# Kernel optimization log

Hardware: AMD Instinct MI355X
Metric: run time of the kernel (lower is better)

The kernel has to match this reference:

```python
import jax, jax.numpy as jnp
import numpy as np

T, B, H = 1024, 128, 256


def setup_inputs() -> dict:
    key = jax.random.key(0)
    k1, k2, k3, k4, k5 = jax.random.split(key, 5)
    ins = jax.random.normal(k1, (T, B, H), dtype=jnp.float32)
    resets = jax.random.randint(k2, (T, B), 0, 2).astype(jnp.bool_)
    # GRUCell params (flax layout): input dense (with bias) and recurrent dense
    # (bias only on the candidate 'hn' branch). Orthogonal-ish init approximated
    # by scaled normal for a pure-jnp reference.
    s = 1.0 / np.sqrt(H)
    Wi = jax.random.normal(k3, (H, 3 * H), dtype=jnp.float32) * s   # -> [ir|iz|in]
    Wh = jax.random.normal(k4, (H, 3 * H), dtype=jnp.float32) * s   # -> [hr|hz|hn]
    bi = jnp.zeros((3 * H,), dtype=jnp.float32)
    bhn = jnp.zeros((H,), dtype=jnp.float32)
    h0 = jnp.zeros((B, H), dtype=jnp.float32)  # initialize_carry -> zeros
    return {"ins": ins, "resets": resets, "h0": h0,
            "Wi": Wi, "Wh": Wh, "bi": bi, "bhn": bhn}


def reference(ins, resets, h0, Wi, Wh, bi, bhn):
    """ScannedRNN: GRU recurrence over time with per-step reset masking.

    ins: [T,B,H], resets: [T,B] bool, h0: [B,H]. Returns (final_carry, ys).
    """
    Hh = h0.shape[-1]

    def step(h, xt):
        x_t, r_t = xt                              # [B,H], [B]
        h = jnp.where(r_t[:, None], 0.0, h)        # reset carry to zeros
        gi = x_t @ Wi + bi                         # [B,3H]
        gh = h @ Wh                                # [B,3H]
        i_r, i_z, i_n = gi[:, :Hh], gi[:, Hh:2 * Hh], gi[:, 2 * Hh:]
        h_r, h_z, h_n = gh[:, :Hh], gh[:, Hh:2 * Hh], gh[:, 2 * Hh:]
        r = jax.nn.sigmoid(i_r + h_r)
        z = jax.nn.sigmoid(i_z + h_z)
        n = jnp.tanh(i_n + r * (h_n + bhn))
        h_new = (1.0 - z) * n + z * h
        return h_new, h_new                        # GRUCell returns (carry, y=carry)

    h_final, ys = jax.lax.scan(step, h0, (ins, resets))
    return h_final, ys
```

## Files before the change

### kernel.cpp

```cpp
#include <hip/hip_runtime.h>


typedef _Float16 half2_t __attribute__((ext_vector_type(2)));
typedef _Float16 half4_t __attribute__((ext_vector_type(4)));
typedef _Float16 half8_t __attribute__((ext_vector_type(8)));
typedef float f32x4 __attribute__((ext_vector_type(4)));

#define T_DIM 1024
#define B_DIM 128
#define H_DIM 256
#define N3 768
#define NSTREAM 8192
#define ROWS 16

__device__ __forceinline__ int perm_n(int cp) {
  int ublk = cp / 48;
  int rem = cp % 48;
  int g = rem >> 4;
  int u4 = rem & 15;
  return g * 256 + ublk * 16 + u4;
}


__global__ void prep_whb(const float* __restrict__ Wh, unsigned* __restrict__ WhB) {
  int i = blockIdx.x * 256 + threadIdx.x;
  int h = 2 * i;
  int idx = h & 7;
  int lane = (h >> 3) & 63;
  int ntk = h >> 9;
  int nt = ntk % 48;
  int kt = ntk / 48;
  int k = kt * 32 + ((lane >> 4) * 8) + idx;
  int n = perm_n(nt * 16 + (lane & 15));
  half2_t p;
  p.x = (_Float16)Wh[(size_t)k * N3 + n];
  p.y = (_Float16)Wh[(size_t)(k + 1) * N3 + n];
  WhB[i] = __builtin_bit_cast(unsigned, p);
}

__global__ void prep_witp(const float* __restrict__ Wi, _Float16* __restrict__ WiTp) {
  int i = blockIdx.x * 256 + threadIdx.x;
  int cp = i >> 8;
  int k = i & 255;
  WiTp[(size_t)cp * 256 + k] = (_Float16)Wi[(size_t)k * N3 + perm_n(cp)];
}

__global__ void prep_bip(const float* __restrict__ bi, float* __restrict__ bip) {
  int i = threadIdx.x;
  bip[i] = bi[perm_n(i)];
}

__global__ void init_h(const float* __restrict__ h0, float* __restrict__ h_state) {
  int i = blockIdx.x * 256 + threadIdx.x;
  h_state[i] = h0[i];
}

__global__ __launch_bounds__(256) void conv_a(
    const float* __restrict__ src, _Float16* __restrict__ dst, int n8) {
  int i = blockIdx.x * 256 + threadIdx.x;
  const int stride = gridDim.x * 256;
  for (; i < n8; i += stride) {
    float4 a = ((const float4*)src)[2 * i];
    float4 b = ((const float4*)src)[2 * i + 1];
    half8_t h;
    h[0] = (_Float16)a.x; h[1] = (_Float16)a.y;
    h[2] = (_Float16)a.z; h[3] = (_Float16)a.w;
    h[4] = (_Float16)b.x; h[5] = (_Float16)b.y;
    h[6] = (_Float16)b.z; h[7] = (_Float16)b.w;
    ((half8_t*)dst)[i] = h;
  }
}


__global__ void seg_transpose(const int* __restrict__ resets, int* __restrict__ resT) {
  int i = blockIdx.x * 256 + threadIdx.x;
  int b = i >> 10;
  int t = i & 1023;
  resT[i] = resets[(size_t)t * B_DIM + b];
}

__global__ __launch_bounds__(256) void seg_extract(
    const int* __restrict__ resT, int t0, int steps,
    unsigned* __restrict__ rowsegs, unsigned* __restrict__ rowcnt,
    unsigned* __restrict__ lhist) {
  const int b = blockIdx.x;
  const int tid = threadIdx.x;
  const int lane = tid & 63;
  const int w = tid >> 6;
  const int per = (steps + 255) >> 8;

  __shared__ unsigned short sstartL[1025];
  __shared__ unsigned lcur[1025];
  __shared__ unsigned wsum[4];

  for (int l = tid; l <= steps; l += 256) lcur[l] = 0;

  const int* rrow = resT + (size_t)b * T_DIM + t0;
  int myfirst = tid * per;
  unsigned cnt = 0;
  for (int i = 0; i < per; ++i) {
    int s = myfirst + i;
    if (s < steps && (s == 0 || rrow[s] != 0)) cnt++;
  }
  unsigned pre = cnt;
#pragma unroll
  for (int off = 1; off < 64; off <<= 1) {
    unsigned v = __shfl_up(pre, off);
    if (lane >= off) pre += v;
  }
  if (lane == 63) wsum[w] = pre;
  __syncthreads();
  unsigned wbase = 0, total = 0;
#pragma unroll
  for (int i = 0; i < 4; ++i) {
    if (i < w) wbase += wsum[i];
    total += wsum[i];
  }
  unsigned r = wbase + pre - cnt;
  for (int i = 0; i < per; ++i) {
    int s = myfirst + i;
    if (s < steps && (s == 0 || rrow[s] != 0)) sstartL[r++] = (unsigned short)s;
  }
  if (tid == 0) { sstartL[total] = (unsigned short)steps; rowcnt[b] = total; }
  __syncthreads();

  const unsigned carry0 = (rrow[0] == 0) ? 1u : 0u;
  for (unsigned rr = tid; rr < total; rr += 256) {
    int st = sstartL[rr];
    int len = (int)sstartL[rr + 1] - st;
    unsigned carry = (st == 0) ? carry0 : 0u;
    unsigned rk = atomicAdd(&lcur[len], 1u);
    rowsegs[(size_t)b * T_DIM + rr] =
        (unsigned)st | ((unsigned)len << 10) | (rk << 21) | (carry << 31);
  }
  __syncthreads();
  for (int l = tid; l <= steps; l += 256) lhist[(size_t)l * 128 + b] = lcur[l];
}

__global__ __launch_bounds__(1024) void seg_prefix2(
    const unsigned* __restrict__ lhist, unsigned* __restrict__ rowoff,
    unsigned* __restrict__ cursors, unsigned* __restrict__ Warr,
    unsigned* __restrict__ nseg, int steps) {
  __shared__ unsigned cs[1024];
  __shared__ unsigned cs2[1024];
  const int tid = threadIdx.x;
  const int len = tid + 1;
  unsigned run = 0;
  if (len <= steps) {
    for (int b = 0; b < 128; ++b) {
      rowoff[(size_t)len * 128 + b] = run;
      run += lhist[(size_t)len * 128 + b];
    }
  }
  unsigned own = run;
  unsigned own2 = run * (unsigned)len;
  cs[tid] = own;
  cs2[tid] = own2;
  for (int off = 1; off < 1024; off <<= 1) {
    __syncthreads();
    unsigned v = (tid + off < 1024) ? cs[tid + off] : 0u;
    unsigned v2 = (tid + off < 1024) ? cs2[tid + off] : 0u;
    __syncthreads();
    cs[tid] += v;
    cs2[tid] += v2;
  }
  cursors[len] = cs[tid] - own;
  Warr[len] = cs2[tid] - own2;
  if (tid == 0) *nseg = cs[0];
}

__global__ void seg_scatter2(
    const unsigned* __restrict__ rowsegs, const unsigned* __restrict__ rowcnt,
    const unsigned* __restrict__ rowoff, const unsigned* __restrict__ cursors,
    unsigned* __restrict__ segs) {
  int i = blockIdx.x * 256 + threadIdx.x;
  int b = i >> 10;
  int rr = i & 1023;
  if ((unsigned)rr >= rowcnt[b]) return;
  unsigned rec = rowsegs[i];
  unsigned st = rec & 0x3FF;
  unsigned len = (rec >> 10) & 0x7FF;
  unsigned rk = (rec >> 21) & 0x3FF;
  unsigned carry = rec >> 31;
  unsigned dst = cursors[len] + rowoff[(size_t)len * 128 + b] + rk;
  segs[dst] = st | (len << 10) | ((unsigned)b << 21) | (carry << 28);
}

__global__ void str_mark(
    const unsigned* __restrict__ segs, const unsigned* __restrict__ nseg_p,
    const unsigned* __restrict__ cursors, const unsigned* __restrict__ Warr,
    unsigned* __restrict__ sstart, unsigned* __restrict__ preexS, int Q) {
  unsigned r = blockIdx.x * 256 + threadIdx.x;
  unsigned n = *nseg_p;
  if (r >= n) return;
  unsigned rec = segs[r];
  unsigned len = (rec >> 10) & 0x7FF;
  unsigned pre = Warr[len] + len * (r - cursors[len]);
  unsigned st = pre / (unsigned)Q;
  unsigned stp;
  if (r == 0) {
    sstart[0] = 0; preexS[0] = 0; stp = 0;
  } else {
    unsigned rec2 = segs[r - 1];
    unsigned len2 = (rec2 >> 10) & 0x7FF;
    unsigned pre2 = Warr[len2] + len2 * (r - 1 - cursors[len2]);
    stp = pre2 / (unsigned)Q;
  }
  for (unsigned s = stp + 1; s <= st; ++s) { sstart[s] = r; preexS[s] = pre; }
}

__global__ __launch_bounds__(256) void gi_gemm(
    const _Float16* __restrict__ A16,
    const _Float16* __restrict__ BT,
    const float* __restrict__ bip,
    _Float16* __restrict__ Cout,
    int M) {
  __shared__ _Float16 Al[128 * 32];
  __shared__ _Float16 Bl[128 * 32];
  const int tid = threadIdx.x;
  const int lane = tid & 63;
  const int w = tid >> 6;
  const int wr = w >> 1, wc = w & 1;
  const int m0 = blockIdx.y * 128;
  const int n0 = blockIdx.x * 128;

  const int srow = lane >> 2;
  const int schunk = lane & 3;

  f32x4 acc[4][4] = {};

  for (int ks = 0; ks < 256; ks += 32) {
#pragma unroll
    for (int rr = 0; rr < 2; ++rr) {
      const int row = w * 32 + rr * 16;
      __builtin_amdgcn_global_load_lds(
          (const __attribute__((address_space(1))) void*)
              ((const char*)A16 + ((size_t)(m0 + row + srow) * 256 + ks) * 2 + schunk * 16),
          (__attribute__((address_space(3))) void*)((char*)Al + row * 64),
          16, 0, 0);
      __builtin_amdgcn_global_load_lds(
          (const __attribute__((address_space(1))) void*)
              ((const char*)BT + ((size_t)(n0 + row + srow) * 256 + ks) * 2 + schunk * 16),
          (__attribute__((address_space(3))) void*)((char*)Bl + row * 64),
          16, 0, 0);
    }
    __syncthreads();

    half8_t af[4], bf[4];
#pragma unroll
    for (int m = 0; m < 4; ++m)
      af[m] = *(const half8_t*)&Al[(size_t)(wr * 64 + m * 16 + (lane & 15)) * 32 + (lane >> 4) * 8];
#pragma unroll
    for (int n = 0; n < 4; ++n)
      bf[n] = *(const half8_t*)&Bl[(size_t)(wc * 64 + n * 16 + (lane & 15)) * 32 + (lane >> 4) * 8];
#pragma unroll
    for (int m = 0; m < 4; ++m)
#pragma unroll
      for (int n = 0; n < 4; ++n)
        acc[m][n] = __builtin_amdgcn_mfma_f32_16x16x32_f16(af[m], bf[n], acc[m][n], 0, 0, 0);
    __syncthreads();
  }

#pragma unroll
  for (int m = 0; m < 4; ++m) {
    int row = m0 + wr * 64 + m * 16 + (lane >> 4) * 4;
#pragma unroll
    for (int n = 0; n < 4; ++n) {
      int col = n0 + wc * 64 + n * 16 + (lane & 15);
      float bv = bip[col];
#pragma unroll
      for (int r2 = 0; r2 < 4; ++r2)
        Cout[(size_t)(row + r2) * N3 + col] = (_Float16)(acc[m][n][r2] + bv);
    }
  }
}

__global__ __launch_bounds__(512)
__attribute__((amdgpu_waves_per_eu(1, 4)))
void scan_stream(
    const _Float16* __restrict__ WhB,
    const _Float16* __restrict__ gi,
    const unsigned* __restrict__ segs,
    const unsigned* __restrict__ sstart,
    const unsigned* __restrict__ preexS,
    const unsigned* __restrict__ nseg_ptr,
    const float* __restrict__ bhn,
    const float* __restrict__ h_in,
    float* __restrict__ h_out,
    float* __restrict__ ys,
    float* __restrict__ hfin,
    int t0, int steps, int Q) {
  __shared__ _Float16 h_lds[2][ROWS][264];
  __shared__ _Float16 giL[2][ROWS][776];
  __shared__ unsigned rst[ROWS];
  __shared__ unsigned rowrankL[ROWS];
  __shared__ unsigned rowpwL[ROWS];
  __shared__ unsigned wava[8];

  const int tid = threadIdx.x;
  const int lane = tid & 63;
  const int w = tid >> 6;
  const int sbase = blockIdx.x * ROWS;
  const unsigned nseg = *nseg_ptr;

  if (tid < ROWS) {
    const unsigned st = sbase + tid;
    unsigned r = sstart[st], pw = preexS[st];
    unsigned v = 0u, rk = 0xFFFFFFFFu, rpw0 = 0u;
    if (r < nseg && pw < (st + 1) * (unsigned)Q) {
      unsigned rec = segs[r];
      unsigned len = (rec >> 10) & 0x7FF;
      v = (rec & 0x3FF) | (((rec >> 21) & 0x7F) << 10) | (len << 17) |
          (((rec >> 28) & 1u) << 28);
      rk = r; rpw0 = pw + len;
    }
    rst[tid] = v; rowrankL[tid] = rk; rowpwL[tid] = rpw0;
  }
  if (tid < 8) wava[tid] = 1u;

  half8_t whr[48];
#pragma unroll
  for (int kt = 0; kt < 8; ++kt)
#pragma unroll
    for (int q = 0; q < 6; ++q)
      whr[kt * 6 + q] =
          *(const half8_t*)&WhB[(((size_t)kt * 48 + w * 6 + q) * 64 + lane) * 8];

  __syncthreads();

  unsigned rcur[2], rnxt[2], rrk[2], rpw[2], segnx[2], lim[2];
  unsigned rfr[2];
#pragma unroll
  for (int rr = 0; rr < 2; ++rr) {
    const int row = 2 * w + rr;
    rcur[rr] = rst[row];
    rrk[rr]  = rowrankL[row];
    rpw[rr]  = rowpwL[row];
    lim[rr]  = (unsigned)(sbase + row + 1) * (unsigned)Q;
    unsigned rn2 = rrk[rr] + 1;
    unsigned i2 = (rn2 < nseg) ? rn2 : (nseg - 1);
    segnx[rr] = segs[i2];
  }

#pragma unroll
  for (int rr = 0; rr < 2; ++rr) {
    int row = 2 * w + rr;
    unsigned s = rcur[rr];
    float4 o = make_float4(0.f, 0.f, 0.f, 0.f);
    if (s & (1u << 28))
      o = *(const float4*)&h_in[(size_t)((s >> 10) & 0x7F) * 256 + lane * 4];
    half4_t hv;
    hv.x = (_Float16)o.x; hv.y = (_Float16)o.y;
    hv.z = (_Float16)o.z; hv.w = (_Float16)o.w;
    *(half4_t*)&h_lds[0][row][lane * 4] = hv;
  }

#pragma unroll
  for (int rr = 0; rr < 2; ++rr) {
    const int row = 2 * w + rr;
    const unsigned ss = rcur[rr];
    if ((ss >> 17) & 0x7FF) {
      const char* src = (const char*)(gi +
          ((size_t)(ss & 0x3FF) * B_DIM + ((ss >> 10) & 0x7F)) * N3);
      char* dst = (char*)&giL[0][row][0];
#if __has_builtin(__builtin_amdgcn_global_load_lds)
      __builtin_amdgcn_global_load_lds(
          (const __attribute__((address_space(1))) void*)(src + (size_t)lane * 16),
          (__attribute__((address_space(3))) void*)dst, 16, 0, 0);
      __builtin_amdgcn_global_load_lds(
          (const __attribute__((address_space(1))) void*)(src + 1024 + (size_t)lane * 4),
          (__attribute__((address_space(3))) void*)(dst + 1024), 4, 0, 0);
      __builtin_amdgcn_global_load_lds(
          (const __attribute__((address_space(1))) void*)(src + 1280 + (size_t)lane * 4),
          (__attribute__((address_space(3))) void*)(dst + 1280), 4, 0, 0);
#else
      {
        uint4 a = *(const uint4*)(src + ((size_t)(lane & 31)) * 48);
        uint4 b = *(const uint4*)(src + ((size_t)(lane & 31)) * 48 + 16);
        uint4 c = *(const uint4*)(src + ((size_t)(lane & 31)) * 48 + 32);
        if ((lane >> 5) == 0) {
          char* d2 = dst + ((size_t)(lane & 31)) * 48;
          *(uint4*)(d2) = a; *(uint4*)(d2 + 16) = b; *(uint4*)(d2 + 32) = c;
        }
      }
#endif
    }
  }

  const int r16 = lane & 15;
  const int q4 = (lane >> 4) * 4;
  const int kq8 = (lane >> 4) * 8;
  const int u0 = w * 32 + r16;
  const float bh0 = bhn[u0];
  const float bh1 = bhn[u0 + 16];

  int cur = 0;
  int hc = 0;
  while (true) {
    asm volatile("s_waitcnt vmcnt(0)" ::: "memory");
    asm volatile("s_waitcnt lgkmcnt(0)" ::: "memory");
    __builtin_amdgcn_s_barrier();
    __builtin_amdgcn_sched_barrier(0);

    unsigned alive = 0;
#pragma unroll
    for (int i = 0; i < 8; ++i) alive += wava[i];
    if (!alive) break;

#pragma unroll
    for (int rr = 0; rr < 2; ++rr) {
      const unsigned cs = rcur[rr];
      const unsigned rem = (cs >> 17) & 0x7FF;
      unsigned nx = 0u;
      rfr[rr] = 0u;
      if (rem > 1) {
        nx = ((cs & 0x3FF) + 1) | (cs & (0x7Fu << 10)) | ((rem - 1) << 17);
      } else if (rem == 1) {
        unsigned rn = rrk[rr] + 1;
        unsigned pw = rpw[rr];
        if (rn < nseg && pw < lim[rr]) {
          unsigned rec = segnx[rr];
          unsigned len = (rec >> 10) & 0x7FF;
          nx = (rec & 0x3FF) | (((rec >> 21) & 0x7F) << 10) | (len << 17) |
               (((rec >> 28) & 1u) << 28);
          rrk[rr] = rn; rpw[rr] = pw + len;
          rfr[rr] = 1u;
          unsigned rn2 = rn + 1;
          unsigned i2 = (rn2 < nseg) ? rn2 : (nseg - 1);
          segnx[rr] = segs[i2];
        }
      }
      rnxt[rr] = nx;
    }

#pragma unroll
    for (int rr = 0; rr < 2; ++rr) {
      const int row = 2 * w + rr;
      const unsigned ss = rnxt[rr];
      if ((ss >> 17) & 0x7FF) {
        const char* src = (const char*)(gi +
            ((size_t)(ss & 0x3FF) * B_DIM + ((ss >> 10) & 0x7F)) * N3);
        char* dst = (char*)&giL[cur ^ 1][row][0];
#if __has_builtin(__builtin_amdgcn_global_load_lds)
        __builtin_amdgcn_global_load_lds(
            (const __attribute__((address_space(1))) void*)(src + (size_t)lane * 16),
            (__attribute__((address_space(3))) void*)dst, 16, 0, 0);
        __builtin_amdgcn_global_load_lds(
            (const __attribute__((address_space(1))) void*)(src + 1024 + (size_t)lane * 4),
            (__attribute__((address_space(3))) void*)(dst + 1024), 4, 0, 0);
        __builtin_amdgcn_global_load_lds(
            (const __attribute__((address_space(1))) void*)(src + 1280 + (size_t)lane * 4),
            (__attribute__((address_space(3))) void*)(dst + 1280), 4, 0, 0);
#else
        {
          uint4 a = *(const uint4*)(src + ((size_t)(lane & 31)) * 48);
          uint4 b = *(const uint4*)(src + ((size_t)(lane & 31)) * 48 + 16);
          uint4 c = *(const uint4*)(src + ((size_t)(lane & 31)) * 48 + 32);
          if ((lane >> 5) == 0) {
            char* d2 = dst + ((size_t)(lane & 31)) * 48;
            *(uint4*)(d2) = a; *(uint4*)(d2 + 16) = b; *(uint4*)(d2 + 32) = c;
          }
        }
#endif
      }
    }

    f32x4 acc[6] = {};
#pragma unroll
    for (int kt = 0; kt < 8; ++kt) {
      half8_t afr = *(const half8_t*)&h_lds[hc][r16][kt * 32 + kq8];
#pragma unroll
      for (int q = 0; q < 6; ++q)
        acc[q] = __builtin_amdgcn_mfma_f32_16x16x32_f16(afr, whr[kt * 6 + q], acc[q], 0, 0, 0);
    }

#pragma unroll
    for (int j = 0; j < 2; ++j) {
      const int u = u0 + j * 16;
      const int cb = w * 96 + j * 48 + r16;
      const float bh = j ? bh1 : bh0;
#pragma unroll
      for (int e = 0; e < 4; ++e) {
        const int row = q4 + e;
        if ((rst[row] >> 17) & 0x7FF) {
          const float gr = (float)giL[cur][row][cb];
          const float gz = (float)giL[cur][row][cb + 16];
          const float gn = (float)giL[cur][row][cb + 32];
          const float sigr = 1.f / (1.f + __expf(-(gr + acc[3 * j][e])));
          const float sigz = 1.f / (1.f + __expf(-(gz + acc[3 * j + 1][e])));
          const float narg = gn + sigr * (acc[3 * j + 2][e] + bh);
          const float eo = __expf(-2.f * narg);
          const float nn = 2.f / (1.f + eo) - 1.f;
          const float hold = (float)h_lds[hc][row][u];
          const float hnew = (1.f - sigz) * nn + sigz * hold;
          h_lds[hc ^ 1][row][u] = (_Float16)hnew;
        }
      }
    }

    asm volatile("s_waitcnt lgkmcnt(0)" ::: "memory");
    __builtin_amdgcn_s_barrier();
    __builtin_amdgcn_sched_barrier(0);

    unsigned alv = 0;
#pragma unroll
    for (int rr = 0; rr < 2; ++rr) {
      const int row = 2 * w + rr;
      const unsigned sp = rcur[rr];
      const unsigned rem = (sp >> 17) & 0x7FF;
      if (rem) {
        const int t = sp & 0x3FF;
        const int b = (sp >> 10) & 0x7F;
        half4_t hv = *(const half4_t*)&h_lds[hc ^ 1][row][lane * 4];
        float4 o;
        o.x = (float)hv.x; o.y = (float)hv.y; o.z = (float)hv.z; o.w = (float)hv.w;
        *(float4*)&ys[(((size_t)(t0 + t) * B_DIM + b) * H_DIM) + lane * 4] = o;
        if (rem == 1) {
          if (t == steps - 1) *(float4*)&h_out[(size_t)b * 256 + lane * 4] = o;
          if (t0 + t == T_DIM - 1) *(float4*)&hfin[(size_t)b * 256 + lane * 4] = o;
        }
      }
      if ((rnxt[rr] >> 17) & 0x7FF) alv++;
      rcur[rr] = rnxt[rr];
      if (lane == 0) rst[row] = rnxt[rr];
      if (rfr[rr]) {
        unsigned s = rnxt[rr];
        float4 o2 = make_float4(0.f, 0.f, 0.f, 0.f);
        if (s & (1u << 28))
          o2 = *(const float4*)&h_in[(size_t)((s >> 10) & 0x7F) * 256 + lane * 4];
        half4_t hv2;
        hv2.x = (_Float16)o2.x; hv2.y = (_Float16)o2.y;
        hv2.z = (_Float16)o2.z; hv2.w = (_Float16)o2.w;
        *(half4_t*)&h_lds[hc ^ 1][row][lane * 4] = hv2;
      }
    }
    if (lane == 0) wava[w] = alv;

    cur ^= 1;
    hc ^= 1;
  }
}

extern "C" void kernel_launch(void* const* d_in, const int* in_sizes, int n_in,
                              void* d_out, int out_size, void* d_ws, size_t ws_size,
                              hipStream_t stream) {
  const float* ins    = (const float*)d_in[0];
  const int*   resets = (const int*)d_in[1];
  const float* h0     = (const float*)d_in[2];
  const float* Wi     = (const float*)d_in[3];
  const float* Wh     = (const float*)d_in[4];
  const float* bi     = (const float*)d_in[5];
  const float* bhn    = (const float*)d_in[6];
  float* out  = (float*)d_out;
  float* hfin = out;
  float* ys   = out + B_DIM * H_DIM;

  char* ws = (char*)d_ws;
  unsigned*  WhB     = (unsigned*)(ws + 0);
  _Float16*  WiTp    = (_Float16*)(ws + 393216);
  float*     bip     = (float*)(ws + 786432);
  float*     hA      = (float*)(ws + 789504);
  float*     hB      = (float*)(ws + 920576);
  int*       resT    = (int*)(ws + 1051648);
  unsigned*  rowsegs = (unsigned*)(ws + 1575936);
  unsigned*  rowcnt  = (unsigned*)(ws + 2100224);
  unsigned*  lhist   = (unsigned*)(ws + 2100736);
  unsigned*  rowoff  = (unsigned*)(ws + 2625536);
  unsigned*  cursors = (unsigned*)(ws + 3150336);
  unsigned*  Warr    = (unsigned*)(ws + 3154560);
  unsigned*  nseg    = (unsigned*)(ws + 3158784);
  unsigned*  segs    = (unsigned*)(ws + 3158912);
  unsigned*  sstart  = (unsigned*)(ws + 3683200);
  unsigned*  preexS  = (unsigned*)(ws + 3748736);
  const size_t gi_off = 3814400;

  int CH = T_DIM;
  while (CH > 256) {
    size_t need = gi_off + (size_t)CH * 128 * (N3 + H_DIM) * 2;
    if (need <= ws_size) break;
    CH >>= 1;
  }
  _Float16* gibuf = (_Float16*)(ws + gi_off);
  _Float16* A16   = (_Float16*)(ws + gi_off + (size_t)CH * 128 * N3 * 2);

  prep_whb<<<384, 256, 0, stream>>>(Wh, WhB);
  prep_witp<<<768, 256, 0, stream>>>(Wi, WiTp);
  prep_bip<<<1, 768, 0, stream>>>(bi, bip);
  init_h<<<128, 256, 0, stream>>>(h0, hA);
  seg_transpose<<<512, 256, 0, stream>>>(resets, resT);

  float* hbufs[2] = {hA, hB};
  for (int c = 0, t0 = 0; t0 < T_DIM; ++c, t0 += CH) {
    int steps = (t0 + CH <= T_DIM) ? CH : (T_DIM - t0);
    int M = steps * B_DIM;
    int Q = (M + NSTREAM - 1) / NSTREAM;
    if (Q < 1) Q = 1;

    conv_a<<<2048, 256, 0, stream>>>(ins + (size_t)t0 * B_DIM * H_DIM, A16, M * 32);

    dim3 ggrid(N3 / 128, M / 128);
    gi_gemm<<<ggrid, 256, 0, stream>>>(A16, WiTp, bip, gibuf, M);

    seg_extract<<<128, 256, 0, stream>>>(resT, t0, steps, rowsegs, rowcnt, lhist);
    seg_prefix2<<<1, 1024, 0, stream>>>(lhist, rowoff, cursors, Warr, nseg, steps);
    seg_scatter2<<<512, 256, 0, stream>>>(rowsegs, rowcnt, rowoff, cursors, segs);
    hipMemsetAsync(sstart, 0xFF, 131072, stream);
    str_mark<<<512, 256, 0, stream>>>(segs, nseg, cursors, Warr, sstart, preexS, Q);

    scan_stream<<<NSTREAM / ROWS, 512, 0, stream>>>(
        (const _Float16*)WhB, gibuf, segs, sstart, preexS, nseg, bhn,
        hbufs[c & 1], hbufs[(c + 1) & 1], ys, hfin, t0, steps, Q);
  }
}
```

Measured before the change: 452.1 us.

## Halve scan streams and make per-step loads/stores branch-free with a dump buffer

Halves the number of independent scan streams (NSTREAM 8192→4096), so there are fewer blocks, each walking longer segment chains, and relaxes the occupancy hint to at most 2 waves per EU. Dead rows now issue their gate-input loads from a dummy offset and write their outputs to a per-block scratch dump buffer, which removes per-row branches from the load, gate and store phases. It also waits with vmcnt(2) instead of vmcnt(0), intended to keep some memory operations in flight across the barrier. The trade-off is redundant loads, math and stores for inactive rows, and a possible ordering hazard from the looser wait count.

```diff
diff --git a/kernel.cpp b/kernel.cpp
--- a/kernel.cpp
+++ b/kernel.cpp
@@ -10,7 +10,7 @@
 #define B_DIM 128
 #define H_DIM 256
 #define N3 768
-#define NSTREAM 8192
+#define NSTREAM 4096
 #define ROWS 16
 
 __device__ __forceinline__ int perm_n(int cp) {
@@ -276,7 +276,7 @@
 }
 
 __global__ __launch_bounds__(512)
-__attribute__((amdgpu_waves_per_eu(1, 4)))
+__attribute__((amdgpu_waves_per_eu(1, 2)))
 void scan_stream(
     const _Float16* __restrict__ WhB,
     const _Float16* __restrict__ gi,
@@ -289,6 +289,7 @@
     float* __restrict__ h_out,
     float* __restrict__ ys,
     float* __restrict__ hfin,
+    float* __restrict__ dump,
     int t0, int steps, int Q) {
   __shared__ _Float16 h_lds[2][ROWS][264];
   __shared__ _Float16 giL[2][ROWS][776];
@@ -302,6 +303,7 @@
   const int w = tid >> 6;
   const int sbase = blockIdx.x * ROWS;
   const unsigned nseg = *nseg_ptr;
+  float* dumpb = dump + (size_t)(blockIdx.x & 63) * 4096;
 
   if (tid < ROWS) {
     const unsigned st = sbase + tid;
@@ -359,32 +361,24 @@
   for (int rr = 0; rr < 2; ++rr) {
     const int row = 2 * w + rr;
     const unsigned ss = rcur[rr];
-    if ((ss >> 17) & 0x7FF) {
-      const char* src = (const char*)(gi +
-          ((size_t)(ss & 0x3FF) * B_DIM + ((ss >> 10) & 0x7F)) * N3);
-      char* dst = (char*)&giL[0][row][0];
-#if __has_builtin(__builtin_amdgcn_global_load_lds)
-      __builtin_amdgcn_global_load_lds(
-          (const __attribute__((address_space(1))) void*)(src + (size_t)lane * 16),
-          (__attribute__((address_space(3))) void*)dst, 16, 0, 0);
-      __builtin_amdgcn_global_load_lds(
-          (const __attribute__((address_space(1))) void*)(src + 1024 + (size_t)lane * 4),
-          (__attribute__((address_space(3))) void*)(dst + 1024), 4, 0, 0);
-      __builtin_amdgcn_global_load_lds(
-          (const __attribute__((address_space(1))) void*)(src + 1280 + (size_t)lane * 4),
-          (__attribute__((address_space(3))) void*)(dst + 1280), 4, 0, 0);
-#else
-      {
-        uint4 a = *(const uint4*)(src + ((size_t)(lane & 31)) * 48);
-        uint4 b = *(const uint4*)(src + ((size_t)(lane & 31)) * 48 + 16);
-        uint4 c = *(const uint4*)(src + ((size_t)(lane & 31)) * 48 + 32);
-        if ((lane >> 5) == 0) {
-          char* d2 = dst + ((size_t)(lane & 31)) * 48;
-          *(uint4*)(d2) = a; *(uint4*)(d2 + 16) = b; *(uint4*)(d2 + 32) = c;
-        }
-      }
-#endif
-    }
+    const int live = (int)((ss >> 17) & 0x7FF);
+    const size_t goff = live ? ((size_t)(ss & 0x3FF) * B_DIM + ((ss >> 10) & 0x7F)) * N3 : 0;
+    const char* src = (const char*)(gi + goff);
+    char* dst = (char*)&giL[0][row][0];
+    __builtin_amdgcn_global_load_lds(
+        (const __attribute__((address_space(1))) void*)(src + (size_t)lane * 16),
+        (__attribute__((address_space(3))) void*)dst, 16, 0, 0);
+    __builtin_amdgcn_global_load_lds(
+        (const __attribute__((address_space(1))) void*)(src + 1024 + (size_t)lane * 4),
+        (__attribute__((address_space(3))) void*)(dst + 1024), 4, 0, 0);
+    __builtin_amdgcn_global_load_lds(
+        (const __attribute__((address_space(1))) void*)(src + 1280 + (size_t)lane * 4),
+        (__attribute__((address_space(3))) void*)(dst + 1280), 4, 0, 0);
+  }
+#pragma unroll
+  for (int rr = 0; rr < 2; ++rr) {
+    const int row = 2 * w + rr;
+    *(float4*)&dumpb[row * 256 + lane * 4] = make_float4(0.f, 0.f, 0.f, 0.f);
   }
 
   const int r16 = lane & 15;
@@ -397,7 +391,7 @@
   int cur = 0;
   int hc = 0;
   while (true) {
-    asm volatile("s_waitcnt vmcnt(0)" ::: "memory");
+    asm volatile("s_waitcnt vmcnt(2)" ::: "memory");
     asm volatile("s_waitcnt lgkmcnt(0)" ::: "memory");
     __builtin_amdgcn_s_barrier();
     __builtin_amdgcn_sched_barrier(0);
@@ -437,32 +431,19 @@
     for (int rr = 0; rr < 2; ++rr) {
       const int row = 2 * w + rr;
       const unsigned ss = rnxt[rr];
-      if ((ss >> 17) & 0x7FF) {
-        const char* src = (const char*)(gi +
-            ((size_t)(ss & 0x3FF) * B_DIM + ((ss >> 10) & 0x7F)) * N3);
-        char* dst = (char*)&giL[cur ^ 1][row][0];
-#if __has_builtin(__builtin_amdgcn_global_load_lds)
-        __builtin_amdgcn_global_load_lds(
-            (const __attribute__((address_space(1))) void*)(src + (size_t)lane * 16),
-            (__attribute__((address_space(3))) void*)dst, 16, 0, 0);
-        __builtin_amdgcn_global_load_lds(
-            (const __attribute__((address_space(1))) void*)(src + 1024 + (size_t)lane * 4),
-            (__attribute__((address_space(3))) void*)(dst + 1024), 4, 0, 0);
-        __builtin_amdgcn_global_load_lds(
-            (const __attribute__((address_space(1))) void*)(src + 1280 + (size_t)lane * 4),
-            (__attribute__((address_space(3))) void*)(dst + 1280), 4, 0, 0);
-#else
-        {
-          uint4 a = *(const uint4*)(src + ((size_t)(lane & 31)) * 48);
-          uint4 b = *(const uint4*)(src + ((size_t)(lane & 31)) * 48 + 16);
-          uint4 c = *(const uint4*)(src + ((size_t)(lane & 31)) * 48 + 32);
-          if ((lane >> 5) == 0) {
-            char* d2 = dst + ((size_t)(lane & 31)) * 48;
-            *(uint4*)(d2) = a; *(uint4*)(d2 + 16) = b; *(uint4*)(d2 + 32) = c;
-          }
-        }
-#endif
-      }
+      const int live = (int)((ss >> 17) & 0x7FF);
+      const size_t goff = live ? ((size_t)(ss & 0x3FF) * B_DIM + ((ss >> 10) & 0x7F)) * N3 : 0;
+      const char* src = (const char*)(gi + goff);
+      char* dst = (char*)&giL[cur ^ 1][row][0];
+      __builtin_amdgcn_global_load_lds(
+          (const __attribute__((address_space(1))) void*)(src + (size_t)lane * 16),
+          (__attribute__((address_space(3))) void*)dst, 16, 0, 0);
+      __builtin_amdgcn_global_load_lds(
+          (const __attribute__((address_space(1))) void*)(src + 1024 + (size_t)lane * 4),
+          (__attribute__((address_space(3))) void*)(dst + 1024), 4, 0, 0);
+      __builtin_amdgcn_global_load_lds(
+          (const __attribute__((address_space(1))) void*)(src + 1280 + (size_t)lane * 4),
+          (__attribute__((address_space(3))) void*)(dst + 1280), 4, 0, 0);
     }
 
     f32x4 acc[6] = {};
@@ -482,19 +463,17 @@
 #pragma unroll
       for (int e = 0; e < 4; ++e) {
         const int row = q4 + e;
-        if ((rst[row] >> 17) & 0x7FF) {
-          const float gr = (float)giL[cur][row][cb];
-          const float gz = (float)giL[cur][row][cb + 16];
-          const float gn = (float)giL[cur][row][cb + 32];
-          const float sigr = 1.f / (1.f + __expf(-(gr + acc[3 * j][e])));
-          const float sigz = 1.f / (1.f + __expf(-(gz + acc[3 * j + 1][e])));
-          const float narg = gn + sigr * (acc[3 * j + 2][e] + bh);
-          const float eo = __expf(-2.f * narg);
-          const float nn = 2.f / (1.f + eo) - 1.f;
-          const float hold = (float)h_lds[hc][row][u];
-          const float hnew = (1.f - sigz) * nn + sigz * hold;
-          h_lds[hc ^ 1][row][u] = (_Float16)hnew;
-        }
+        const float gr = (float)giL[cur][row][cb];
+        const float gz = (float)giL[cur][row][cb + 16];
+        const float gn = (float)giL[cur][row][cb + 32];
+        const float sigr = 1.f / (1.f + __expf(-(gr + acc[3 * j][e])));
+        const float sigz = 1.f / (1.f + __expf(-(gz + acc[3 * j + 1][e])));
+        const float narg = gn + sigr * (acc[3 * j + 2][e] + bh);
+        const float eo = __expf(-2.f * narg);
+        const float nn = 2.f / (1.f + eo) - 1.f;
+        const float hold = (float)h_lds[hc][row][u];
+        const float hnew = (1.f - sigz) * nn + sigz * hold;
+        h_lds[hc ^ 1][row][u] = (_Float16)hnew;
       }
     }
 
@@ -508,21 +487,21 @@
       const int row = 2 * w + rr;
       const unsigned sp = rcur[rr];
       const unsigned rem = (sp >> 17) & 0x7FF;
-      if (rem) {
-        const int t = sp & 0x3FF;
-        const int b = (sp >> 10) & 0x7F;
-        half4_t hv = *(const half4_t*)&h_lds[hc ^ 1][row][lane * 4];
-        float4 o;
-        o.x = (float)hv.x; o.y = (float)hv.y; o.z = (float)hv.z; o.w = (float)hv.w;
-        *(float4*)&ys[(((size_t)(t0 + t) * B_DIM + b) * H_DIM) + lane * 4] = o;
-        if (rem == 1) {
-          if (t == steps - 1) *(float4*)&h_out[(size_t)b * 256 + lane * 4] = o;
-          if (t0 + t == T_DIM - 1) *(float4*)&hfin[(size_t)b * 256 + lane * 4] = o;
-        }
+      const int t = sp & 0x3FF;
+      const int b = (sp >> 10) & 0x7F;
+      half4_t hv = *(const half4_t*)&h_lds[hc ^ 1][row][lane * 4];
+      float4 o;
+      o.x = (float)hv.x; o.y = (float)hv.y; o.z = (float)hv.z; o.w = (float)hv.w;
+      float* ydst = rem
+          ? &ys[(((size_t)(t0 + t) * B_DIM + b) * H_DIM) + lane * 4]
+          : &dumpb[row * 256 + lane * 4];
+      *(float4*)ydst = o;
+      if (rem == 1) {
+        if (t == steps - 1) *(float4*)&h_out[(size_t)b * 256 + lane * 4] = o;
+        if (t0 + t == T_DIM - 1) *(float4*)&hfin[(size_t)b * 256 + lane * 4] = o;
       }
       if ((rnxt[rr] >> 17) & 0x7FF) alv++;
       rcur[rr] = rnxt[rr];
-      if (lane == 0) rst[row] = rnxt[rr];
       if (rfr[rr]) {
         unsigned s = rnxt[rr];
         float4 o2 = make_float4(0.f, 0.f, 0.f, 0.f);
@@ -572,7 +551,8 @@
   unsigned*  segs    = (unsigned*)(ws + 3158912);
   unsigned*  sstart  = (unsigned*)(ws + 3683200);
   unsigned*  preexS  = (unsigned*)(ws + 3748736);
-  const size_t gi_off = 3814400;
+  float*     dump    = (float*)(ws + 3814400);
+  const size_t gi_off = 4862976;
 
   int CH = T_DIM;
   while (CH > 256) {
@@ -609,6 +589,6 @@
 
     scan_stream<<<NSTREAM / ROWS, 512, 0, stream>>>(
         (const _Float16*)WhB, gibuf, segs, sstart, preexS, nseg, bhn,
-        hbufs[c & 1], hbufs[(c + 1) & 1], ys, hfin, t0, steps, Q);
-  }
-}
+        hbufs[c & 1], hbufs[(c + 1) & 1], ys, hfin, dump, t0, steps, Q);
+  }
+}
```

Result: faster. 413.9 us (-8.4%).
